# Kernel tuning notes

Measured on AMD Instinct MI355X. Metric: run time of the kernel, lower is better.

Reference implementation:

```python
import jax, jax.numpy as jnp
import numpy as np

B, S, D = 2, 2048, 2560
H, KVH, HD = 8, 4, 256
N_REP = H // KVH
SCALING = 256 ** -0.5
SOFTCAP = 50.0
WINDOW = 512
EPS = 1e-6
NEG = -1e9


def _rope_cos_sin(seq_len, dim, base=10000.0):
    inv_freq = 1.0 / (base ** (jnp.arange(0, dim, 2, dtype=jnp.float32) / dim))
    t = jnp.arange(seq_len, dtype=jnp.float32)
    freqs = jnp.outer(t, inv_freq)              # [S, dim/2]
    emb = jnp.concatenate([freqs, freqs], -1)   # [S, dim]
    return jnp.cos(emb), jnp.sin(emb)


def setup_inputs() -> dict:
    key = jax.random.key(0)
    ks = jax.random.split(key, 6)
    hidden_states = jax.random.normal(ks[0], (B, S, D), jnp.float32)
    cos1, sin1 = _rope_cos_sin(S, HD)
    cos = jnp.broadcast_to(cos1[None], (B, S, HD)).astype(jnp.float32)
    sin = jnp.broadcast_to(sin1[None], (B, S, HD)).astype(jnp.float32)
    # sliding-window causal additive mask [1,1,S,S]
    i = jnp.arange(S)[:, None]
    j = jnp.arange(S)[None, :]
    ok = (j <= i) & ((i - j) < WINDOW)
    attention_mask = jnp.where(ok, 0.0, NEG).astype(jnp.float32)[None, None]
    scale = 0.02
    q_w = jax.random.normal(ks[1], (H * HD, D), jnp.float32) * scale
    k_w = jax.random.normal(ks[2], (KVH * HD, D), jnp.float32) * scale
    v_w = jax.random.normal(ks[3], (KVH * HD, D), jnp.float32) * scale
    o_w = jax.random.normal(ks[4], (D, H * HD), jnp.float32) * scale
    q_norm_w = jnp.zeros((HD,), jnp.float32)
    k_norm_w = jnp.zeros((HD,), jnp.float32)
    return {"hidden_states": hidden_states, "cos": cos, "sin": sin,
            "attention_mask": attention_mask, "q_w": q_w, "k_w": k_w,
            "v_w": v_w, "o_w": o_w, "q_norm_w": q_norm_w, "k_norm_w": k_norm_w}


def _rms_norm(x, w):
    xf = x.astype(jnp.float32)
    n = xf * jax.lax.rsqrt(jnp.mean(xf * xf, -1, keepdims=True) + EPS)
    return (n * (1.0 + w.astype(jnp.float32))).astype(x.dtype)


def _rotate_half(x):
    x1, x2 = jnp.split(x, 2, axis=-1)
    return jnp.concatenate([-x2, x1], -1)


def reference(hidden_states, cos, sin, attention_mask, q_w, k_w, v_w, o_w,
              q_norm_w, k_norm_w):
    b, s, _ = hidden_states.shape
    # projections -> [B, heads, S, HD]
    q = (hidden_states @ q_w.T).reshape(b, s, H, HD).transpose(0, 2, 1, 3)
    k = (hidden_states @ k_w.T).reshape(b, s, KVH, HD).transpose(0, 2, 1, 3)
    v = (hidden_states @ v_w.T).reshape(b, s, KVH, HD).transpose(0, 2, 1, 3)
    q = _rms_norm(q, q_norm_w)
    k = _rms_norm(k, k_norm_w)
    c = cos[:, None]  # [B,1,S,HD]
    sn = sin[:, None]
    q = q * c + _rotate_half(q) * sn
    k = k * c + _rotate_half(k) * sn
    # GQA repeat
    k = jnp.repeat(k, N_REP, axis=1)
    v = jnp.repeat(v, N_REP, axis=1)
    scores = jnp.einsum('bhqd,bhkd->bhqk', q, k) * SCALING
    scores = SOFTCAP * jnp.tanh(scores / SOFTCAP)
    scores = scores + attention_mask[:, :, :, :s]
    probs = jax.nn.softmax(scores.astype(jnp.float32), axis=-1).astype(q.dtype)
    out = jnp.einsum('bhqk,bhkd->bhqd', probs, v)
    out = out.transpose(0, 2, 1, 3).reshape(b, s, H * HD)
    attn_output = out @ o_w.T
    return attn_output, probs
```

## Files before the change

kernel.cpp:

```cpp
#include <hip/hip_runtime.h>

typedef _Float16 f16;
typedef float f32x4 __attribute__((ext_vector_type(4)));
typedef _Float16 f16x8 __attribute__((ext_vector_type(8)));
typedef _Float16 f16x4 __attribute__((ext_vector_type(4)));
typedef _Float16 f16x2 __attribute__((ext_vector_type(2)));

#define MFMA16(a, b, c) __builtin_amdgcn_mfma_f32_16x16x32_f16((a), (b), (c), 0, 0, 0)

__device__ __forceinline__ void gld16(const void* g, void* l) {
    __builtin_amdgcn_global_load_lds((const __attribute__((address_space(1))) unsigned int*)g,
                                     (__attribute__((address_space(3))) unsigned int*)l, 16, 0, 0);
}

__global__ __launch_bounds__(256) void cvt_all(const float* __restrict__ hs, const float* __restrict__ qw,
                                               const float* __restrict__ kw, const float* __restrict__ vw,
                                               const float* __restrict__ ow, f16* __restrict__ hsb,
                                               f16* __restrict__ wqkv, f16* __restrict__ owb) {
    long g = (long)(blockIdx.x * 256 + threadIdx.x) * 8;
    const float* src;
    f16* dst;
    long off;
    if (g < 10485760L) { src = hs; dst = hsb; off = g; }
    else if (g < 15728640L) { src = qw; dst = wqkv; off = g - 10485760L; }
    else if (g < 18350080L) { src = kw; dst = wqkv + 5242880; off = g - 15728640L; }
    else if (g < 20971520L) { src = vw; dst = wqkv + 7864320; off = g - 18350080L; }
    else { src = ow; dst = owb; off = g - 20971520L; }
    float4 a = *(const float4*)(src + off);
    float4 b = *(const float4*)(src + off + 4);
    f16x8 o;
    o[0] = (f16)a.x; o[1] = (f16)a.y; o[2] = (f16)a.z; o[3] = (f16)a.w;
    o[4] = (f16)b.x; o[5] = (f16)b.y; o[6] = (f16)b.z; o[7] = (f16)b.w;
    *(f16x8*)(dst + off) = o;
}

template <int K, int N, int GN, bool F16OUT>
__global__ __launch_bounds__(512, 1) void gemm256(const f16* __restrict__ A, const f16* __restrict__ W,
                                                  void* __restrict__ Cv) {
    constexpr int NT = K / 32;
    __shared__ __align__(16) char lds[131072];
    const int tid = threadIdx.x;
    const int lane = tid & 63, wid = tid >> 6;
    const int wr = wid >> 2, wc = wid & 3;
    int bid = blockIdx.x;
    int swz = (bid & 7) * ((16 * GN) >> 3) + (bid >> 3);
    const int m0 = (swz / GN) * 256, n0 = (swz % GN) * 256;

    const int kel = 8 * ((tid & 3) ^ ((tid >> 2) & 3));
    const f16* pA0 = A + (size_t)(m0 + (tid >> 2)) * K + kel;
    const f16* pA1 = pA0 + (size_t)128 * K;
    const f16* pB0 = W + (size_t)(n0 + (tid >> 2)) * K + kel;
    const f16* pB1 = pB0 + (size_t)128 * K;
    const int dst_o = tid * 16;

#define QSTAGE(bi, t)                                                     \
    {                                                                     \
        char* ab_ = lds + (bi) * 32768;                                   \
        int k0_ = (t) * 32;                                               \
        gld16(pA0 + k0_, ab_ + dst_o);                                    \
        gld16(pA1 + k0_, ab_ + 8192 + dst_o);                             \
        gld16(pB0 + k0_, ab_ + 16384 + dst_o);                            \
        gld16(pB1 + k0_, ab_ + 24576 + dst_o);                            \
    }

    const int ccx = (((lane >> 4) << 4) ^ ((lane & 3) << 4));
    const int ar = wr * 128 + (lane & 15);
    const int br = wc * 64 + (lane & 15);

    f32x4 acc[8][4] = {};

#define QCOMPUTE(bi)                                                      \
    {                                                                     \
        const char* ab_ = lds + (bi) * 32768;                             \
        const char* bb_ = ab_ + 16384;                                    \
        f16x8 Af[8], Bf[4];                                               \
        _Pragma("unroll")                                                 \
        for (int m = 0; m < 8; ++m)                                       \
            Af[m] = *(const f16x8*)(ab_ + (ar + m * 16) * 64 + ccx);      \
        _Pragma("unroll")                                                 \
        for (int n = 0; n < 4; ++n)                                       \
            Bf[n] = *(const f16x8*)(bb_ + (br + n * 16) * 64 + ccx);      \
        __builtin_amdgcn_s_setprio(1);                                    \
        _Pragma("unroll")                                                 \
        for (int m = 0; m < 8; ++m)                                       \
            _Pragma("unroll")                                             \
            for (int n = 0; n < 4; ++n)                                   \
                acc[m][n] = MFMA16(Af[m], Bf[n], acc[m][n]);              \
        __builtin_amdgcn_s_setprio(0);                                    \
    }

    QSTAGE(0, 0)
    QSTAGE(1, 1)
    QSTAGE(2, 2)
    asm volatile("s_waitcnt vmcnt(8)" ::: "memory");
    __builtin_amdgcn_s_barrier();

#pragma unroll 1
    for (int t = 0; t < NT - 3; ++t) {
        QCOMPUTE(t & 3)
        asm volatile("s_waitcnt lgkmcnt(0)" ::: "memory");
        __builtin_amdgcn_s_barrier();
        QSTAGE((t + 3) & 3, t + 3)
        asm volatile("s_waitcnt vmcnt(8)" ::: "memory");
        __builtin_amdgcn_s_barrier();
    }
    QCOMPUTE((NT - 3) & 3)
    asm volatile("s_waitcnt lgkmcnt(0)" ::: "memory");
    __builtin_amdgcn_s_barrier();
    asm volatile("s_waitcnt vmcnt(4)" ::: "memory");
    __builtin_amdgcn_s_barrier();
    QCOMPUTE((NT - 2) & 3)
    asm volatile("s_waitcnt lgkmcnt(0)" ::: "memory");
    __builtin_amdgcn_s_barrier();
    asm volatile("s_waitcnt vmcnt(0)" ::: "memory");
    __builtin_amdgcn_s_barrier();
    QCOMPUTE((NT - 1) & 3)

#pragma unroll
    for (int m = 0; m < 8; ++m) {
        int row = m0 + wr * 128 + m * 16 + ((lane >> 4) << 2);
#pragma unroll
        for (int n = 0; n < 4; ++n) {
            int col = n0 + wc * 64 + n * 16 + (lane & 15);
#pragma unroll
            for (int r = 0; r < 4; ++r) {
                if constexpr (F16OUT)
                    ((f16*)Cv)[(size_t)(row + r) * N + col] = (f16)acc[m][n][r];
                else
                    ((float*)Cv)[(size_t)(row + r) * N + col] = acc[m][n][r];
            }
        }
    }
#undef QSTAGE
#undef QCOMPUTE
}

__global__ __launch_bounds__(256) void rmsrope_k(const f16* __restrict__ qkvh,
                                                 const float* __restrict__ cosb, const float* __restrict__ sinb,
                                                 const float* __restrict__ qnw, const float* __restrict__ knw,
                                                 f16* __restrict__ qr, f16* __restrict__ kr) {
    int wid = threadIdx.x >> 6, lane = threadIdx.x & 63;
    int task = blockIdx.x * 4 + wid;
    int slot = task % 12;
    int bs = task / 12;
    int b = bs >> 11, s = bs & 2047;
    const f16* src;
    const float* w;
    f16* dst;
    if (slot < 8) {
        src = qkvh + (size_t)bs * 4096 + slot * 256;
        w = qnw;
        dst = qr + ((size_t)(b * 8 + slot) * 2048 + s) * 256;
    } else {
        int h = slot - 8;
        src = qkvh + (size_t)bs * 4096 + 2048 + h * 256;
        w = knw;
        dst = kr + ((size_t)(b * 4 + h) * 2048 + s) * 256;
    }
    int i = lane * 4;
    f16x4 xr = *(const f16x4*)(src + i);
    float4 x;
    x.x = (float)xr[0]; x.y = (float)xr[1]; x.z = (float)xr[2]; x.w = (float)xr[3];
    float ss = x.x * x.x + x.y * x.y + x.z * x.z + x.w * x.w;
#pragma unroll
    for (int o = 32; o; o >>= 1) ss += __shfl_xor(ss, o, 64);
    float rs = rsqrtf(ss * (1.0f / 256.0f) + 1e-6f);
    float4 y;
    y.x = __shfl_xor(x.x, 32, 64);
    y.y = __shfl_xor(x.y, 32, 64);
    y.z = __shfl_xor(x.z, 32, 64);
    y.w = __shfl_xor(x.w, 32, 64);
    float4 wv = *(const float4*)(w + i);
    float4 wp = *(const float4*)(w + (i ^ 128));
    float4 c = *(const float4*)(cosb + (size_t)bs * 256 + i);
    float4 sn = *(const float4*)(sinb + (size_t)bs * 256 + i);
    float sgn = (lane < 32) ? -1.0f : 1.0f;
    float n0 = x.x * rs * (1.f + wv.x), n1 = x.y * rs * (1.f + wv.y);
    float n2 = x.z * rs * (1.f + wv.z), n3 = x.w * rs * (1.f + wv.w);
    float r0 = y.x * rs * (1.f + wp.x) * sgn, r1 = y.y * rs * (1.f + wp.y) * sgn;
    float r2 = y.z * rs * (1.f + wp.z) * sgn, r3 = y.w * rs * (1.f + wp.w) * sgn;
    float o0 = n0 * c.x + r0 * sn.x;
    float o1 = n1 * c.y + r1 * sn.y;
    float o2 = n2 * c.z + r2 * sn.z;
    float o3 = n3 * c.w + r3 * sn.w;
    f16x4 outv;
    outv[0] = (f16)o0; outv[1] = (f16)o1; outv[2] = (f16)o2; outv[3] = (f16)o3;
    *(f16x4*)(dst + i) = outv;
}

__global__ __launch_bounds__(256) void vtrans2(const f16* __restrict__ qkvh, f16* __restrict__ vt) {
    __shared__ __align__(16) char Ls[64 * 516];
    int tile = blockIdx.x;
    int st = tile & 31;
    int by = tile >> 5;
    int b = by >> 2, kvh = by & 3;
    int tid = threadIdx.x;
    int s0 = st * 64;
    const f16* src = qkvh + ((size_t)(b * 2048 + s0)) * 4096 + 3072 + kvh * 256;
#pragma unroll
    for (int it = 0; it < 8; ++it) {
        int idx = it * 256 + tid;
        int srow = idx >> 5;
        int col8 = (idx & 31) * 8;
        f16x8 x = *(const f16x8*)(src + (size_t)srow * 4096 + col8);
        char* lp = Ls + srow * 516 + col8 * 2;
        *(f16x2*)(lp)      = f16x2{x[0], x[1]};
        *(f16x2*)(lp + 4)  = f16x2{x[2], x[3]};
        *(f16x2*)(lp + 8)  = f16x2{x[4], x[5]};
        *(f16x2*)(lp + 12) = f16x2{x[6], x[7]};
    }
    __syncthreads();
    f16* dst = vt + ((size_t)(by * 256) * 2048) + s0;
#pragma unroll
    for (int p = 0; p < 8; ++p) {
        int d = p * 32 + (tid >> 3);
        int s8 = (tid & 7) * 8;
        f16x8 o;
#pragma unroll
        for (int j = 0; j < 8; ++j)
            o[j] = *(const f16*)(Ls + (s8 + j) * 516 + d * 2);
        *(f16x8*)(dst + (size_t)d * 2048 + s8) = o;
    }
}

__global__ __launch_bounds__(256) void attn_fused(const f16* __restrict__ qr, const f16* __restrict__ kr,
                                                  const f16* __restrict__ vt, float* __restrict__ probs,
                                                  f16* __restrict__ attn) {
    int qt = blockIdx.x, bh = blockIdx.y;
    int b = bh >> 3, h = bh & 7;
    int tid = threadIdx.x, lane = tid & 63, w = tid >> 6;
    int g = lane >> 4;
    __shared__ __align__(16) char lds[73728];
    char* plb = lds + 65536;

    const f16* qbase = qr + ((size_t)bh * 2048 + qt * 64 + w * 16 + (lane & 15)) * 256 + g * 8;
    f16x8 af[8];
#pragma unroll
    for (int ks = 0; ks < 8; ++ks) af[ks] = *(const f16x8*)(qbase + ks * 32);

    const int kt_first = (qt >= 8) ? 0 : (8 - qt);
    const f16* kb0 = kr + ((size_t)((b * 4 + (h >> 1)) * 2048)) * 256;

#define KSTAGE(kta_, par_)                                                    \
    {                                                                         \
        const f16* kb_ = kb0 + (size_t)(kta_) * 16384;                        \
        char* db_ = lds + (par_) * 32768;                                     \
        _Pragma("unroll")                                                     \
        for (int is = 0; is < 8; ++is) {                                      \
            int off = is * 4096 + w * 1024 + lane * 16;                       \
            int row = off >> 9;                                               \
            int sb = (off & 511) ^ ((row & 7) << 4);                          \
            gld16(kb_ + row * 256 + (sb >> 1), db_ + off);                    \
        }                                                                     \
    }

    KSTAGE(qt - 8 + kt_first, kt_first & 1)
    f32x4 acc[9][4] = {};
#pragma unroll
    for (int kt = 0; kt < 9; ++kt) {
        int kta = qt - 8 + kt;
        if (kta >= 0) {
            if (kt < 8) {
                KSTAGE(kta + 1, (kt + 1) & 1)
                asm volatile("s_waitcnt vmcnt(8)" ::: "memory");
            } else {
                asm volatile("s_waitcnt vmcnt(0)" ::: "memory");
            }
            __builtin_amdgcn_s_barrier();
            __builtin_amdgcn_sched_barrier(0);
            const char* kbuf = lds + (kt & 1) * 32768;
            __builtin_amdgcn_s_setprio(1);
#pragma unroll
            for (int n = 0; n < 4; ++n) {
                int row2 = n * 16 + (lane & 15);
#pragma unroll
                for (int ks = 0; ks < 8; ++ks) {
                    int cb = (ks * 64 + g * 16) ^ ((row2 & 7) << 4);
                    f16x8 bfr = *(const f16x8*)(kbuf + row2 * 512 + cb);
                    acc[kt][n] = MFMA16(af[ks], bfr, acc[kt][n]);
                }
            }
            __builtin_amdgcn_s_setprio(0);
            __builtin_amdgcn_s_barrier();
        }
    }

    int row_l = w * 16 + (g << 2);
    int row_g0 = qt * 64 + row_l;
    f32x4 mx = {-1e30f, -1e30f, -1e30f, -1e30f};
#pragma unroll
    for (int kt = 0; kt < 9; ++kt) {
        int kta = qt - 8 + kt;
#pragma unroll
        for (int n = 0; n < 4; ++n) {
            int col = kta * 64 + n * 16 + (lane & 15);
#pragma unroll
            for (int r = 0; r < 4; ++r) {
                float s = acc[kt][n][r] * 0.0625f;
                float t = __expf(s * 0.04f);
                float v = 50.0f * (t - 1.0f) / (t + 1.0f);
                int rowg = row_g0 + r;
                bool ok = (kta >= 0) && (col <= rowg) && (rowg - col < 512);
                float pv_ = ok ? v : -1e9f;
                acc[kt][n][r] = pv_;
                mx[r] = fmaxf(mx[r], pv_);
            }
        }
    }
#pragma unroll
    for (int o = 1; o < 16; o <<= 1) {
#pragma unroll
        for (int r = 0; r < 4; ++r) mx[r] = fmaxf(mx[r], __shfl_xor(mx[r], o, 64));
    }
    f32x4 sm = {0.f, 0.f, 0.f, 0.f};
#pragma unroll
    for (int kt = 0; kt < 9; ++kt)
#pragma unroll
        for (int n = 0; n < 4; ++n)
#pragma unroll
            for (int r = 0; r < 4; ++r) {
                float e = __expf(acc[kt][n][r] - mx[r]);
                acc[kt][n][r] = e;
                sm[r] += e;
            }
#pragma unroll
    for (int o = 1; o < 16; o <<= 1) {
#pragma unroll
        for (int r = 0; r < 4; ++r) sm[r] += __shfl_xor(sm[r], o, 64);
    }
    f32x4 inv;
#pragma unroll
    for (int r = 0; r < 4; ++r) inv[r] = 1.0f / sm[r];
    f16x4 ph[9][4];
#pragma unroll
    for (int kt = 0; kt < 9; ++kt)
#pragma unroll
        for (int n = 0; n < 4; ++n)
#pragma unroll
            for (int r = 0; r < 4; ++r)
                ph[kt][n][r] = (f16)(acc[kt][n][r] * inv[r]);

    const f16* vtb = vt + (size_t)((b * 4 + (h >> 1)) * 256) * 2048;

#define VSTAGE(kta_, par_)                                                    \
    {                                                                         \
        char* db_ = lds + (par_) * 32768;                                     \
        _Pragma("unroll")                                                     \
        for (int is = 0; is < 8; ++is) {                                      \
            int off = is * 4096 + w * 1024 + lane * 16;                       \
            int d = off >> 7;                                                 \
            int sb = (off & 127) ^ ((d & 7) << 4);                            \
            gld16(vtb + (size_t)d * 2048 + (kta_) * 64 + (sb >> 1), db_ + off); \
        }                                                                     \
    }

    VSTAGE(qt - 8 + kt_first, kt_first & 1)
    f32x4 pacc[16] = {};
#pragma unroll
    for (int kt = 0; kt < 9; ++kt) {
        int kta = qt - 8 + kt;
        if (kta >= 0) {
            if (kt < 8) VSTAGE(kta + 1, (kt + 1) & 1)
#pragma unroll
            for (int n = 0; n < 4; ++n)
#pragma unroll
                for (int r = 0; r < 4; ++r) {
                    int row = row_l + r;
                    int cb = (n * 16 + (lane & 15)) * 2;
                    *(f16*)(plb + row * 128 + (cb ^ ((row & 7) << 4))) = ph[kt][n][r];
                }
            if (kt < 8) {
                asm volatile("s_waitcnt vmcnt(8) lgkmcnt(0)" ::: "memory");
            } else {
                asm volatile("s_waitcnt vmcnt(0) lgkmcnt(0)" ::: "memory");
            }
            __builtin_amdgcn_s_barrier();
            __builtin_amdgcn_sched_barrier(0);
#pragma unroll
            for (int n = 0; n < 4; ++n) {
                int col = kta * 64 + n * 16 + (lane & 15);
#pragma unroll
                for (int r = 0; r < 4; ++r)
                    probs[((size_t)bh * 2048 + row_g0 + r) * 2048 + col] = (float)ph[kt][n][r];
            }
            const char* vbuf = lds + (kt & 1) * 32768;
            int rowp = w * 16 + (lane & 15);
            int pswz = (rowp & 7) << 4;
            f16x8 a0 = *(const f16x8*)(plb + rowp * 128 + ((g * 16) ^ pswz));
            f16x8 a1 = *(const f16x8*)(plb + rowp * 128 + ((g * 16 + 64) ^ pswz));
            __builtin_amdgcn_s_setprio(1);
#pragma unroll
            for (int n = 0; n < 16; ++n) {
                int d = n * 16 + (lane & 15);
                int vswz = (d & 7) << 4;
                f16x8 b0 = *(const f16x8*)(vbuf + d * 128 + ((g * 16) ^ vswz));
                f16x8 b1 = *(const f16x8*)(vbuf + d * 128 + ((g * 16 + 64) ^ vswz));
                pacc[n] = MFMA16(a0, b0, pacc[n]);
                pacc[n] = MFMA16(a1, b1, pacc[n]);
            }
            __builtin_amdgcn_s_setprio(0);
            __builtin_amdgcn_s_barrier();
        }
    }
#undef KSTAGE
#undef VSTAGE

    int kt0 = qt > 8 ? qt - 8 : 0;
    int pre = kt0 * 64;
    int suf = (qt + 1) * 64;
    float4 z4 = make_float4(0.f, 0.f, 0.f, 0.f);
    for (int r = 0; r < 16; ++r) {
        float* rp = probs + ((size_t)bh * 2048 + qt * 64 + w * 16 + r) * 2048;
        for (int off = lane * 4; off < pre; off += 256) *(float4*)(rp + off) = z4;
        for (int off = suf + lane * 4; off < 2048; off += 256) *(float4*)(rp + off) = z4;
    }

    size_t obase = ((size_t)b * 2048 + qt * 64 + row_l) * 2048 + h * 256;
#pragma unroll
    for (int n = 0; n < 16; ++n) {
        int col = n * 16 + (lane & 15);
#pragma unroll
        for (int r = 0; r < 4; ++r)
            attn[obase + (size_t)r * 2048 + col] = (f16)pacc[n][r];
    }
}

extern "C" void kernel_launch(void* const* d_in, const int* in_sizes, int n_in,
                              void* d_out, int out_size, void* d_ws, size_t ws_size,
                              hipStream_t stream) {
    (void)in_sizes; (void)n_in; (void)out_size; (void)ws_size;
    const float* hs   = (const float*)d_in[0];
    const float* cosb = (const float*)d_in[1];
    const float* sinb = (const float*)d_in[2];
    const float* qw   = (const float*)d_in[4];
    const float* kw   = (const float*)d_in[5];
    const float* vw   = (const float*)d_in[6];
    const float* ow   = (const float*)d_in[7];
    const float* qnw  = (const float*)d_in[8];
    const float* knw  = (const float*)d_in[9];

    float* out = (float*)d_out;
    float* probs = out + (size_t)2 * 2048 * 2560;

    char* ws = (char*)d_ws;
    f16* hsb  = (f16*)(ws);
    f16* wqkv = (f16*)(ws + 20971520);
    f16* owb  = (f16*)(ws + 41943040);
    f16* qkvh = (f16*)(ws + 52428800);
    f16* qr   = (f16*)(ws + 85983232);
    f16* kr   = (f16*)(ws + 102760448);
    f16* vt   = (f16*)(ws + 111149056);
    f16* attn = (f16*)(ws + 119537664);

    cvt_all<<<12800, 256, 0, stream>>>(hs, qw, kw, vw, ow, hsb, wqkv, owb);

    gemm256<2560, 4096, 16, true><<<256, 512, 0, stream>>>(hsb, wqkv, qkvh);

    rmsrope_k<<<12288, 256, 0, stream>>>(qkvh, cosb, sinb, qnw, knw, qr, kr);
    vtrans2<<<256, 256, 0, stream>>>(qkvh, vt);

    attn_fused<<<dim3(32, 16), 256, 0, stream>>>(qr, kr, vt, probs, attn);

    gemm256<2048, 2560, 10, false><<<160, 512, 0, stream>>>(attn, owb, out);
}
```

Before: 343.9 us.

## Use 64-wide K tiles with double buffering in the GEMM kernel

The GEMM mainloop now loads 64-element K slices per stage (64KB of LDS per stage) with an 8-way XOR swizzle, replacing 32-element slices. The four-stage pipeline is replaced by a simple two-stage double buffer that issues the next stage before computing the current one, then waits for everything and barriers once per iteration. This halves the number of barriers and loop iterations. In exchange the prefetch distance drops from three stages to one, so global load latency is less well hidden.

```diff
diff --git a/kernel.cpp b/kernel.cpp
--- a/kernel.cpp
+++ b/kernel.cpp
@@ -37,84 +37,77 @@
 template <int K, int N, int GN, bool F16OUT>
 __global__ __launch_bounds__(512, 1) void gemm256(const f16* __restrict__ A, const f16* __restrict__ W,
                                                   void* __restrict__ Cv) {
-    constexpr int NT = K / 32;
+    constexpr int NT = K / 64;
     __shared__ __align__(16) char lds[131072];
     const int tid = threadIdx.x;
     const int lane = tid & 63, wid = tid >> 6;
     const int wr = wid >> 2, wc = wid & 3;
+    const int g = lane >> 4;
     int bid = blockIdx.x;
     int swz = (bid & 7) * ((16 * GN) >> 3) + (bid >> 3);
     const int m0 = (swz / GN) * 256, n0 = (swz % GN) * 256;
 
-    const int kel = 8 * ((tid & 3) ^ ((tid >> 2) & 3));
-    const f16* pA0 = A + (size_t)(m0 + (tid >> 2)) * K + kel;
-    const f16* pA1 = pA0 + (size_t)128 * K;
-    const f16* pB0 = W + (size_t)(n0 + (tid >> 2)) * K + kel;
-    const f16* pB1 = pB0 + (size_t)128 * K;
+    const int kel = 8 * ((tid & 7) ^ ((tid >> 3) & 7));
+    const int rowb = tid >> 3;
+    const f16* pA = A + (size_t)(m0 + rowb) * K + kel;
+    const f16* pB = W + (size_t)(n0 + rowb) * K + kel;
     const int dst_o = tid * 16;
 
 #define QSTAGE(bi, t)                                                     \
     {                                                                     \
-        char* ab_ = lds + (bi) * 32768;                                   \
-        int k0_ = (t) * 32;                                               \
-        gld16(pA0 + k0_, ab_ + dst_o);                                    \
-        gld16(pA1 + k0_, ab_ + 8192 + dst_o);                             \
-        gld16(pB0 + k0_, ab_ + 16384 + dst_o);                            \
-        gld16(pB1 + k0_, ab_ + 24576 + dst_o);                            \
-    }
-
-    const int ccx = (((lane >> 4) << 4) ^ ((lane & 3) << 4));
-    const int ar = wr * 128 + (lane & 15);
-    const int br = wc * 64 + (lane & 15);
+        char* lb_ = lds + (bi) * 65536;                                   \
+        int k0_ = (t) * 64;                                               \
+        gld16(pA + k0_,                 lb_ + dst_o);                     \
+        gld16(pA + (size_t)64 * K + k0_,  lb_ + 8192 + dst_o);            \
+        gld16(pA + (size_t)128 * K + k0_, lb_ + 16384 + dst_o);           \
+        gld16(pA + (size_t)192 * K + k0_, lb_ + 24576 + dst_o);           \
+        gld16(pB + k0_,                 lb_ + 32768 + dst_o);             \
+        gld16(pB + (size_t)64 * K + k0_,  lb_ + 40960 + dst_o);           \
+        gld16(pB + (size_t)128 * K + k0_, lb_ + 49152 + dst_o);           \
+        gld16(pB + (size_t)192 * K + k0_, lb_ + 57344 + dst_o);           \
+    }
+
+    const int xorv = (lane & 7) << 4;
+    const int arow = wr * 128 + (lane & 15);
+    const int brow = wc * 64 + (lane & 15);
 
     f32x4 acc[8][4] = {};
 
 #define QCOMPUTE(bi)                                                      \
     {                                                                     \
-        const char* ab_ = lds + (bi) * 32768;                             \
-        const char* bb_ = ab_ + 16384;                                    \
-        f16x8 Af[8], Bf[4];                                               \
+        const char* ab_ = lds + (bi) * 65536;                             \
+        const char* bb_ = ab_ + 32768;                                    \
         _Pragma("unroll")                                                 \
-        for (int m = 0; m < 8; ++m)                                       \
-            Af[m] = *(const f16x8*)(ab_ + (ar + m * 16) * 64 + ccx);      \
-        _Pragma("unroll")                                                 \
-        for (int n = 0; n < 4; ++n)                                       \
-            Bf[n] = *(const f16x8*)(bb_ + (br + n * 16) * 64 + ccx);      \
-        __builtin_amdgcn_s_setprio(1);                                    \
-        _Pragma("unroll")                                                 \
-        for (int m = 0; m < 8; ++m)                                       \
+        for (int ks = 0; ks < 2; ++ks) {                                  \
+            const int cc = (ks * 64 + g * 16) ^ xorv;                     \
+            f16x8 Af[8], Bf[4];                                           \
+            _Pragma("unroll")                                             \
+            for (int m = 0; m < 8; ++m)                                   \
+                Af[m] = *(const f16x8*)(ab_ + (arow + m * 16) * 128 + cc);\
             _Pragma("unroll")                                             \
             for (int n = 0; n < 4; ++n)                                   \
-                acc[m][n] = MFMA16(Af[m], Bf[n], acc[m][n]);              \
-        __builtin_amdgcn_s_setprio(0);                                    \
+                Bf[n] = *(const f16x8*)(bb_ + (brow + n * 16) * 128 + cc);\
+            __builtin_amdgcn_s_setprio(1);                                \
+            _Pragma("unroll")                                             \
+            for (int m = 0; m < 8; ++m)                                   \
+                _Pragma("unroll")                                         \
+                for (int n = 0; n < 4; ++n)                               \
+                    acc[m][n] = MFMA16(Af[m], Bf[n], acc[m][n]);          \
+            __builtin_amdgcn_s_setprio(0);                                \
+        }                                                                 \
     }
 
     QSTAGE(0, 0)
-    QSTAGE(1, 1)
-    QSTAGE(2, 2)
-    asm volatile("s_waitcnt vmcnt(8)" ::: "memory");
-    __builtin_amdgcn_s_barrier();
-
-#pragma unroll 1
-    for (int t = 0; t < NT - 3; ++t) {
-        QCOMPUTE(t & 3)
-        asm volatile("s_waitcnt lgkmcnt(0)" ::: "memory");
-        __builtin_amdgcn_s_barrier();
-        QSTAGE((t + 3) & 3, t + 3)
-        asm volatile("s_waitcnt vmcnt(8)" ::: "memory");
-        __builtin_amdgcn_s_barrier();
-    }
-    QCOMPUTE((NT - 3) & 3)
-    asm volatile("s_waitcnt lgkmcnt(0)" ::: "memory");
-    __builtin_amdgcn_s_barrier();
-    asm volatile("s_waitcnt vmcnt(4)" ::: "memory");
-    __builtin_amdgcn_s_barrier();
-    QCOMPUTE((NT - 2) & 3)
-    asm volatile("s_waitcnt lgkmcnt(0)" ::: "memory");
-    __builtin_amdgcn_s_barrier();
     asm volatile("s_waitcnt vmcnt(0)" ::: "memory");
     __builtin_amdgcn_s_barrier();
-    QCOMPUTE((NT - 1) & 3)
+
+#pragma unroll 1
+    for (int t = 0; t < NT; ++t) {
+        if (t + 1 < NT) QSTAGE((t + 1) & 1, t + 1)
+        QCOMPUTE(t & 1)
+        asm volatile("s_waitcnt vmcnt(0) lgkmcnt(0)" ::: "memory");
+        __builtin_amdgcn_s_barrier();
+    }
 
 #pragma unroll
     for (int m = 0; m < 8; ++m) {
```

Result: faster. 323.2 us (-6.0%).
